# Kernel optimization log

Measured on AMD Instinct MI355X. Metric: run time of the kernel, lower is better.

## Reference

```python
import jax, jax.numpy as jnp
import numpy as np

PS = 7        # patch (window) size
DIM = 192     # channels
HEADS = 8
HID = 768     # mlp hidden = 4*dim
B = 8
HH = 112
WW = 112
EPS = 1e-5


def _rel_pos_index(ps):
    coords = np.stack(np.meshgrid(np.arange(ps), np.arange(ps), indexing='ij'))
    cf = coords.reshape(2, -1)
    rel = (cf[:, :, None] - cf[:, None, :]).transpose(1, 2, 0).astype(np.int64)
    rel[:, :, 0] += ps - 1
    rel[:, :, 1] += ps - 1
    rel[:, :, 0] *= 2 * ps - 1
    return rel.sum(-1)  # (N, N)

REL_IDX = jnp.asarray(_rel_pos_index(PS))  # (49, 49) int


def layer_norm(x, g, b):
    m = jnp.mean(x, axis=-1, keepdims=True)
    v = jnp.var(x, axis=-1, keepdims=True)
    return (x - m) * jax.lax.rsqrt(v + EPS) * g + b


def setup_inputs() -> dict:
    key = jax.random.key(0)
    ks = jax.random.split(key, 8)
    s = 0.02
    return {
        'x': jax.random.normal(ks[0], (B, HH * WW, DIM), jnp.float32),
        'norm1_g': jnp.ones((DIM,), jnp.float32),
        'norm1_b': jnp.zeros((DIM,), jnp.float32),
        'q_w': jax.random.normal(ks[1], (DIM, DIM), jnp.float32) * s,
        'q_b': jnp.zeros((DIM,), jnp.float32),
        'kv_w': jax.random.normal(ks[2], (2 * DIM, DIM), jnp.float32) * s,
        'kv_b': jnp.zeros((2 * DIM,), jnp.float32),
        'rpe_table': jax.random.normal(ks[3], ((2 * PS - 1) ** 2, HEADS), jnp.float32) * s,
        'proj_w': jax.random.normal(ks[4], (DIM, DIM), jnp.float32) * s,
        'proj_b': jnp.zeros((DIM,), jnp.float32),
        'norm2_g': jnp.ones((DIM,), jnp.float32),
        'norm2_b': jnp.zeros((DIM,), jnp.float32),
        'fc1_w': jax.random.normal(ks[5], (HID, DIM), jnp.float32) * s,
        'fc1_b': jnp.zeros((HID,), jnp.float32),
        'dw_w': jax.random.normal(ks[6], (HID, 1, 3, 3), jnp.float32) * s,
        'dw_b': jnp.zeros((HID,), jnp.float32),
        'fc2_w': jax.random.normal(ks[7], (DIM, HID), jnp.float32) * s,
        'fc2_b': jnp.zeros((DIM,), jnp.float32),
        'H': HH,
        'W': WW,
    }


def reference(x, norm1_g, norm1_b, q_w, q_b, kv_w, kv_b, rpe_table,
              proj_w, proj_b, norm2_g, norm2_b, fc1_w, fc1_b, dw_w, dw_b,
              fc2_w, fc2_b, H, W):
    Bsz, L, C = x.shape
    N = PS * PS
    hd = C // HEADS
    scale = hd ** -0.5
    nh, nw = H // PS, W // PS  # H, W chosen divisible by PS -> no padding

    shortcut = x
    xn = layer_norm(x, norm1_g, norm1_b)
    xi = xn.reshape(Bsz, H, W, C)
    # partition into non-overlapping PS x PS windows: (B*nP, N, C)
    p = xi.reshape(Bsz, nh, PS, nw, PS, C).transpose(0, 1, 3, 2, 4, 5).reshape(-1, N, C)

    # IPSA window attention (memory == x, T = 1)
    q = (p @ q_w.T + q_b).reshape(-1, N, HEADS, hd).transpose(0, 2, 1, 3) * scale
    kv = (p @ kv_w.T + kv_b).reshape(-1, N, 2, HEADS, hd).transpose(2, 0, 3, 1, 4)
    k, v = kv[0], kv[1]  # (B_, heads, N, hd)
    attn = jnp.einsum('bhnd,bhmd->bhnm', q, k)
    bias = rpe_table[REL_IDX.reshape(-1)].reshape(N, N, HEADS).transpose(2, 0, 1)
    attn = jax.nn.softmax(attn + bias[None], axis=-1)
    out = jnp.einsum('bhnm,bhmd->bhnd', attn, v).transpose(0, 2, 1, 3).reshape(-1, N, C)
    out = out @ proj_w.T + proj_b
    # reverse window partition back to (B, L, C)
    out = out.reshape(Bsz, nh, nw, PS, PS, C).transpose(0, 1, 3, 2, 4, 5).reshape(Bsz, L, C)
    x = shortcut + out

    # MLP with depthwise conv
    y = layer_norm(x, norm2_g, norm2_b)
    y = y @ fc1_w.T + fc1_b  # (B, L, HID)
    yc = y.transpose(0, 2, 1).reshape(Bsz, HID, H, W)
    yc = jax.lax.conv_general_dilated(
        yc, dw_w, window_strides=(1, 1), padding=((1, 1), (1, 1)),
        dimension_numbers=('NCHW', 'OIHW', 'NCHW'), feature_group_count=HID,
    ) + dw_b[None, :, None, None]
    y = yc.reshape(Bsz, HID, L).transpose(0, 2, 1)
    y = jax.nn.gelu(y, approximate=False)
    y = y @ fc2_w.T + fc2_b
    return x + y
```

## Files before the change

### kernel.cpp

```cpp
#include <hip/hip_runtime.h>
#include <hip/hip_bf16.h>
#include <cmath>

#define C_DIM 192
#define HID 768

typedef __attribute__((ext_vector_type(8))) __bf16 bf16x8;
typedef __attribute__((ext_vector_type(4))) float f32x4;

__device__ __forceinline__ void gload_lds16(const void* g, void* l) {
  __builtin_amdgcn_global_load_lds(
      (__attribute__((address_space(1))) void*)(const_cast<void*>(g)),
      (__attribute__((address_space(3))) void*)(l), 16, 0, 0);
}

__device__ __forceinline__ float bfu2f(ushort u) {
  return __uint_as_float((unsigned)u << 16);
}
__device__ __forceinline__ ushort f2bfu(float f) {
  __hip_bfloat16 h = __float2bfloat16(f);
  return *reinterpret_cast<ushort*>(&h);
}
__device__ __forceinline__ float fgelu(float x) {
  float z = x * (1.5957691216f + 0.071354816f * x * x);
  return x / (1.f + __expf(-z));
}

__global__ __launch_bounds__(256) void prep_kernel(
    const float* __restrict__ q_w, const float* __restrict__ q_b,
    const float* __restrict__ kv_w, const float* __restrict__ kv_b,
    const float* __restrict__ proj_w, const float* __restrict__ fc1_w,
    const float* __restrict__ fc2_w,
    __hip_bfloat16* __restrict__ wcat, float* __restrict__ bcat,
    __hip_bfloat16* __restrict__ projw, __hip_bfloat16* __restrict__ fc1w,
    __hip_bfloat16* __restrict__ fc2w)
{
  int idx = blockIdx.x * 256 + threadIdx.x;
  const float scale = 0.20412414523193154f;
  if (idx < 110592) {
    float v = (idx < 36864) ? q_w[idx] * scale : kv_w[idx - 36864];
    wcat[idx] = __float2bfloat16(v);
  }
  if (idx < 576) bcat[idx] = (idx < 192) ? q_b[idx] * scale : kv_b[idx - 192];
  if (idx < 36864) projw[idx] = __float2bfloat16(proj_w[idx]);
  if (idx < 147456) {
    fc1w[idx] = __float2bfloat16(fc1_w[idx]);
    fc2w[idx] = __float2bfloat16(fc2_w[idx]);
  }
}

__global__ __launch_bounds__(256) void ln_kernel(
    const float* __restrict__ x, const float* __restrict__ g,
    const float* __restrict__ b, __hip_bfloat16* __restrict__ out)
{
  int t = blockIdx.x * 4 + (threadIdx.x >> 6);
  int lane = threadIdx.x & 63;
  const float* xr = x + (size_t)t * C_DIM;
  float v0 = xr[lane], v1 = xr[lane + 64], v2 = xr[lane + 128];
  float s = v0 + v1 + v2;
  float sq = v0 * v0 + v1 * v1 + v2 * v2;
  #pragma unroll
  for (int off = 32; off > 0; off >>= 1) {
    s += __shfl_xor(s, off, 64);
    sq += __shfl_xor(sq, off, 64);
  }
  float mean = s * (1.0f / 192.0f);
  float var = sq * (1.0f / 192.0f) - mean * mean;
  float rstd = rsqrtf(var + 1e-5f);
  size_t o = (size_t)t * C_DIM;
  out[o + lane]       = __float2bfloat16((v0 - mean) * rstd * g[lane] + b[lane]);
  out[o + lane + 64]  = __float2bfloat16((v1 - mean) * rstd * g[lane + 64] + b[lane + 64]);
  out[o + lane + 128] = __float2bfloat16((v2 - mean) * rstd * g[lane + 128] + b[lane + 128]);
}

template <int EPI>
__global__ __launch_bounds__(256) void gemmA_kernel(
    const ushort* __restrict__ X, int lda, const ushort* __restrict__ W,
    const float* __restrict__ bias, const float* __restrict__ addin,
    void* __restrict__ outp, int N)
{
  __shared__ __align__(16) ushort Al[128 * 192];
  __shared__ __align__(16) ushort Bl[64 * 192];
  const int tid = threadIdx.x;
  const int lane = tid & 63;
  const int wv = tid >> 6;
  const int quad = lane >> 4;
  const int m15 = lane & 15;
  const long mBase = (long)blockIdx.y * 128;
  const int NT = N >> 6;

  #pragma unroll
  for (int r = 0; r < 12; ++r) {
    int sI = tid + r * 256;
    int row = sI / 24;
    int cs = sI - row * 24;
    int gc = cs - (row % 24); if (gc < 0) gc += 24;
    gload_lds16(X + (mBase + row) * (long)lda + gc * 8, Al + sI * 8);
  }

  const int rA0 = wv * 32 + m15, rA1 = rA0 + 16;
  const int rA0m = rA0 % 24, rA1m = rA1 % 24;

  for (int nt = 0; nt < NT; ++nt) {
    __syncthreads();
    #pragma unroll
    for (int r = 0; r < 6; ++r) {
      int sI = tid + r * 256;
      int row = sI / 24;
      int cs = sI - row * 24;
      int gc = cs - (row % 24); if (gc < 0) gc += 24;
      gload_lds16(W + (long)(nt * 64 + row) * 192 + gc * 8, Bl + sI * 8);
    }
    __syncthreads();

    f32x4 acc[2][4];
    #pragma unroll
    for (int r = 0; r < 2; ++r)
      #pragma unroll
      for (int c = 0; c < 4; ++c) acc[r][c] = (f32x4){0.f, 0.f, 0.f, 0.f};

    #pragma unroll
    for (int ks = 0; ks < 6; ++ks) {
      const int l = ks * 4 + quad;
      int pa0 = l + rA0m; if (pa0 >= 24) pa0 -= 24;
      int pa1 = l + rA1m; if (pa1 >= 24) pa1 -= 24;
      bf16x8 a0 = *(const bf16x8*)&Al[rA0 * 192 + pa0 * 8];
      bf16x8 a1 = *(const bf16x8*)&Al[rA1 * 192 + pa1 * 8];
      #pragma unroll
      for (int ct = 0; ct < 4; ++ct) {
        const int rB = ct * 16 + m15;
        int pb = l + (rB % 24); if (pb >= 24) pb -= 24;
        bf16x8 b = *(const bf16x8*)&Bl[rB * 192 + pb * 8];
        acc[0][ct] = __builtin_amdgcn_mfma_f32_16x16x32_bf16(a0, b, acc[0][ct], 0, 0, 0);
        acc[1][ct] = __builtin_amdgcn_mfma_f32_16x16x32_bf16(a1, b, acc[1][ct], 0, 0, 0);
      }
    }
    #pragma unroll
    for (int rt = 0; rt < 2; ++rt)
      #pragma unroll
      for (int ct = 0; ct < 4; ++ct)
        #pragma unroll
        for (int i = 0; i < 4; ++i) {
          long row = mBase + wv * 32 + rt * 16 + quad * 4 + i;
          int col = nt * 64 + ct * 16 + m15;
          float v = acc[rt][ct][i] + bias[col];
          if (EPI == 1) {
            v += addin[row * N + col];
            ((float*)outp)[row * N + col] = v;
          } else {
            ((__hip_bfloat16*)outp)[row * N + col] = __float2bfloat16(v);
          }
        }
  }
}

__global__ __launch_bounds__(256) void gemmB_kernel(
    const ushort* __restrict__ X, const ushort* __restrict__ W,
    const float* __restrict__ bias, const float* __restrict__ addin,
    float* __restrict__ outp)
{
  __shared__ __align__(16) ushort Al[128 * 192];
  __shared__ __align__(16) ushort Bl[64 * 192];
  const int tid = threadIdx.x;
  const int lane = tid & 63;
  const int wv = tid >> 6;
  const int quad = lane >> 4;
  const int m15 = lane & 15;
  const long mBase = (long)blockIdx.y * 128;

  const int rA0 = wv * 32 + m15, rA1 = rA0 + 16;
  const int rA0m = rA0 % 24, rA1m = rA1 % 24;

  f32x4 acc[3][2][4];
  #pragma unroll
  for (int n = 0; n < 3; ++n)
    #pragma unroll
    for (int r = 0; r < 2; ++r)
      #pragma unroll
      for (int c = 0; c < 4; ++c) acc[n][r][c] = (f32x4){0.f, 0.f, 0.f, 0.f};

  for (int kc = 0; kc < 4; ++kc) {
    for (int nt = 0; nt < 3; ++nt) {
      __syncthreads();
      if (nt == 0) {
        #pragma unroll
        for (int r = 0; r < 12; ++r) {
          int sI = tid + r * 256;
          int row = sI / 24;
          int cs = sI - row * 24;
          int gc = cs - (row % 24); if (gc < 0) gc += 24;
          gload_lds16(X + (mBase + row) * 768l + kc * 192 + gc * 8, Al + sI * 8);
        }
      }
      #pragma unroll
      for (int r = 0; r < 6; ++r) {
        int sI = tid + r * 256;
        int row = sI / 24;
        int cs = sI - row * 24;
        int gc = cs - (row % 24); if (gc < 0) gc += 24;
        gload_lds16(W + (long)(nt * 64 + row) * 768 + kc * 192 + gc * 8, Bl + sI * 8);
      }
      __syncthreads();
      #pragma unroll
      for (int ks = 0; ks < 6; ++ks) {
        const int l = ks * 4 + quad;
        int pa0 = l + rA0m; if (pa0 >= 24) pa0 -= 24;
        int pa1 = l + rA1m; if (pa1 >= 24) pa1 -= 24;
        bf16x8 a0 = *(const bf16x8*)&Al[rA0 * 192 + pa0 * 8];
        bf16x8 a1 = *(const bf16x8*)&Al[rA1 * 192 + pa1 * 8];
        #pragma unroll
        for (int ct = 0; ct < 4; ++ct) {
          const int rB = ct * 16 + m15;
          int pb = l + (rB % 24); if (pb >= 24) pb -= 24;
          bf16x8 b = *(const bf16x8*)&Bl[rB * 192 + pb * 8];
          acc[nt][0][ct] = __builtin_amdgcn_mfma_f32_16x16x32_bf16(a0, b, acc[nt][0][ct], 0, 0, 0);
          acc[nt][1][ct] = __builtin_amdgcn_mfma_f32_16x16x32_bf16(a1, b, acc[nt][1][ct], 0, 0, 0);
        }
      }
    }
  }
  #pragma unroll
  for (int nt = 0; nt < 3; ++nt)
    #pragma unroll
    for (int rt = 0; rt < 2; ++rt)
      #pragma unroll
      for (int ct = 0; ct < 4; ++ct)
        #pragma unroll
        for (int i = 0; i < 4; ++i) {
          long row = mBase + wv * 32 + rt * 16 + quad * 4 + i;
          int col = nt * 64 + ct * 16 + m15;
          float v = acc[nt][rt][ct][i] + bias[col] + addin[row * 192 + col];
          outp[row * 192 + col] = v;
        }
}

__global__ __launch_bounds__(256) void attn_kernel(
    const float* __restrict__ rpe, __hip_bfloat16* __restrict__ qkv)
{
  __shared__ float lds[4 * 2352 + 4 * 172];
  const int tid = threadIdx.x;
  const int lane = tid & 63;
  const int wv = tid >> 6;
  const int wh = blockIdx.x * 4 + wv;
  const int h = wh & 7;
  const int win = wh >> 3;
  const int b = win >> 8;
  const int wl = win & 255;
  const int whi = wl >> 4;
  const int wwi = wl & 15;
  ushort* qkv_u = (ushort*)qkv;
  float* kv_w = &lds[wv * 2352];
  float* bias_w = &lds[4 * 2352 + wv * 172];

  const long rowbase = (long)b * 12544 + (long)(whi * 7) * 112 + wwi * 7;

  #pragma unroll
  for (int rnd = 0; rnd < 10; ++rnd) {
    int e = lane + rnd * 64;
    if (e < 588) {
      int t = e / 12;
      int r = e - t * 12;
      int mat = r / 6;
      int d4 = (r - mat * 6) * 4;
      int py = t / 7, px = t - py * 7;
      long row = rowbase + py * 112 + px;
      ushort4 u = *(const ushort4*)(qkv_u + row * 576 + 192 + mat * 192 + h * 24 + d4);
      float* dst = kv_w + mat * 1176 + t * 24 + d4;
      dst[0] = bfu2f(u.x); dst[1] = bfu2f(u.y);
      dst[2] = bfu2f(u.z); dst[3] = bfu2f(u.w);
    }
  }
  for (int r = lane; r < 169; r += 64) bias_w[r] = rpe[r * 8 + h];
  __syncthreads();

  const int i = (lane < 49) ? lane : 48;
  const int yi = i / 7, xi = i - yi * 7;
  const int base_i = yi * 13 + xi + 84;
  const long myrow = rowbase + yi * 112 + xi;

  float q[24];
  #pragma unroll
  for (int d4 = 0; d4 < 24; d4 += 4) {
    ushort4 u = *(const ushort4*)(qkv_u + myrow * 576 + h * 24 + d4);
    q[d4] = bfu2f(u.x); q[d4 + 1] = bfu2f(u.y);
    q[d4 + 2] = bfu2f(u.z); q[d4 + 3] = bfu2f(u.w);
  }

  float s[49];
  #pragma unroll
  for (int j = 0; j < 49; ++j) {
    const int yj = j / 7, xj = j % 7;
    const int base_j = yj * 13 + xj;
    const float* kr = kv_w + j * 24;
    float acc = 0.f;
    #pragma unroll
    for (int d4 = 0; d4 < 24; d4 += 4) {
      f32x4 kk = *(const f32x4*)(kr + d4);
      acc += q[d4] * kk[0] + q[d4 + 1] * kk[1] + q[d4 + 2] * kk[2] + q[d4 + 3] * kk[3];
    }
    s[j] = acc + bias_w[base_i - base_j];
  }

  float mx = s[0];
  #pragma unroll
  for (int j = 1; j < 49; ++j) mx = fmaxf(mx, s[j]);
  float sm = 0.f;
  #pragma unroll
  for (int j = 0; j < 49; ++j) { s[j] = __expf(s[j] - mx); sm += s[j]; }
  const float inv = 1.f / sm;
  #pragma unroll
  for (int j = 0; j < 49; ++j) s[j] *= inv;

  float o[24];
  #pragma unroll
  for (int d = 0; d < 24; ++d) o[d] = 0.f;
  #pragma unroll
  for (int j = 0; j < 49; ++j) {
    const float p = s[j];
    const float* vr = kv_w + 1176 + j * 24;
    #pragma unroll
    for (int d4 = 0; d4 < 24; d4 += 4) {
      f32x4 vvv = *(const f32x4*)(vr + d4);
      o[d4] += p * vvv[0]; o[d4 + 1] += p * vvv[1];
      o[d4 + 2] += p * vvv[2]; o[d4 + 3] += p * vvv[3];
    }
  }

  if (lane < 49) {
    #pragma unroll
    for (int d4 = 0; d4 < 24; d4 += 4) {
      ushort4 u;
      u.x = f2bfu(o[d4]); u.y = f2bfu(o[d4 + 1]);
      u.z = f2bfu(o[d4 + 2]); u.w = f2bfu(o[d4 + 3]);
      *(ushort4*)(qkv_u + myrow * 576 + h * 24 + d4) = u;
    }
  }
}

__global__ __launch_bounds__(192) void dwconv_gelu_kernel(
    const ushort* __restrict__ y1, const float* __restrict__ w,
    const float* __restrict__ bias, ushort* __restrict__ y2)
{
  const int c = threadIdx.x * 4;
  const int w0 = blockIdx.y * 2;
  const int b = blockIdx.z;
  const int h0 = blockIdx.x * 28;

  float wt[9][4];
  #pragma unroll
  for (int k = 0; k < 9; ++k)
    #pragma unroll
    for (int j = 0; j < 4; ++j) wt[k][j] = w[(c + j) * 9 + k];
  float bs[4];
  #pragma unroll
  for (int j = 0; j < 4; ++j) bs[j] = bias[c + j];

  const bool okL = (w0 > 0), okR = (w0 + 2 < 112);
  ushort4 rb[6][4];

  auto loadrow = [&](int h, ushort4 dst[4]) {
    const ushort4 z = {0, 0, 0, 0};
    if (h < 0 || h >= 112) {
      dst[0] = z; dst[1] = z; dst[2] = z; dst[3] = z;
      return;
    }
    const ushort* p = y1 + (((size_t)(b * 112 + h)) * 112 + w0) * HID + c;
    dst[0] = okL ? *(const ushort4*)(p - HID) : z;
    dst[1] = *(const ushort4*)(p);
    dst[2] = *(const ushort4*)(p + HID);
    dst[3] = okR ? *(const ushort4*)(p + 2 * HID) : z;
  };

  loadrow(h0 - 1, rb[0]);
  loadrow(h0, rb[1]);

  for (int m = 0; m < 7; ++m) {
    const int hb = h0 + m * 4;
    loadrow(hb + 1, rb[2]);
    loadrow(hb + 2, rb[3]);
    loadrow(hb + 3, rb[4]);
    loadrow(hb + 4, rb[5]);
    #pragma unroll
    for (int o = 0; o < 4; ++o) {
      float acc0[4], acc1[4];
      #pragma unroll
      for (int j = 0; j < 4; ++j) { acc0[j] = bs[j]; acc1[j] = bs[j]; }
      #pragma unroll
      for (int dy = 0; dy < 3; ++dy) {
        float col[4][4];
        #pragma unroll
        for (int x = 0; x < 4; ++x) {
          ushort4 u = rb[o + dy][x];
          col[x][0] = bfu2f(u.x); col[x][1] = bfu2f(u.y);
          col[x][2] = bfu2f(u.z); col[x][3] = bfu2f(u.w);
        }
        #pragma unroll
        for (int dx = 0; dx < 3; ++dx)
          #pragma unroll
          for (int j = 0; j < 4; ++j) {
            acc0[j] += wt[dy * 3 + dx][j] * col[dx][j];
            acc1[j] += wt[dy * 3 + dx][j] * col[dx + 1][j];
          }
      }
      ushort* outp = y2 + (((size_t)(b * 112 + hb + o)) * 112 + w0) * HID + c;
      ushort4 o0, o1;
      o0.x = f2bfu(fgelu(acc0[0])); o0.y = f2bfu(fgelu(acc0[1]));
      o0.z = f2bfu(fgelu(acc0[2])); o0.w = f2bfu(fgelu(acc0[3]));
      o1.x = f2bfu(fgelu(acc1[0])); o1.y = f2bfu(fgelu(acc1[1]));
      o1.z = f2bfu(fgelu(acc1[2])); o1.w = f2bfu(fgelu(acc1[3]));
      *(ushort4*)(outp) = o0;
      *(ushort4*)(outp + HID) = o1;
    }
    #pragma unroll
    for (int x = 0; x < 4; ++x) {
      rb[0][x] = rb[4][x];
      rb[1][x] = rb[5][x];
    }
  }
}

extern "C" void kernel_launch(void* const* d_in, const int* in_sizes, int n_in,
                              void* d_out, int out_size, void* d_ws, size_t ws_size,
                              hipStream_t stream) {
  const float* x      = (const float*)d_in[0];
  const float* n1g    = (const float*)d_in[1];
  const float* n1b    = (const float*)d_in[2];
  const float* q_w    = (const float*)d_in[3];
  const float* q_b    = (const float*)d_in[4];
  const float* kv_w   = (const float*)d_in[5];
  const float* kv_b   = (const float*)d_in[6];
  const float* rpe    = (const float*)d_in[7];
  const float* proj_w = (const float*)d_in[8];
  const float* proj_b = (const float*)d_in[9];
  const float* n2g    = (const float*)d_in[10];
  const float* n2b    = (const float*)d_in[11];
  const float* fc1_w  = (const float*)d_in[12];
  const float* fc1_b  = (const float*)d_in[13];
  const float* dw_w   = (const float*)d_in[14];
  const float* dw_b   = (const float*)d_in[15];
  const float* fc2_w  = (const float*)d_in[16];
  const float* fc2_b  = (const float*)d_in[17];
  float* out = (float*)d_out;

  char* ws = (char*)d_ws;
  __hip_bfloat16* wcat  = (__hip_bfloat16*)(ws);
  __hip_bfloat16* projw = (__hip_bfloat16*)(ws + 221184);
  __hip_bfloat16* fc1w  = (__hip_bfloat16*)(ws + 294912);
  __hip_bfloat16* fc2w  = (__hip_bfloat16*)(ws + 589824);
  float* bcat           = (float*)(ws + 884736);
  const size_t WOFF = 1u << 20;

  int CB = 8;
  while (CB > 1 && WOFF + (size_t)CB * 12544 * 3456 > ws_size) CB >>= 1;
  const size_t Mc = (size_t)CB * 12544;
  char* Abuf = ws + WOFF;
  char* Bbuf = Abuf + Mc * 384;
  char* Cbuf = Bbuf + Mc * 1536;
  __hip_bfloat16* xn  = (__hip_bfloat16*)Abuf;
  __hip_bfloat16* qkv = (__hip_bfloat16*)Bbuf;
  __hip_bfloat16* y2  = (__hip_bfloat16*)Bbuf;
  __hip_bfloat16* y1  = (__hip_bfloat16*)Cbuf;

  prep_kernel<<<576, 256, 0, stream>>>(q_w, q_b, kv_w, kv_b, proj_w, fc1_w,
                                       fc2_w, wcat, bcat, projw, fc1w, fc2w);

  const int nChunks = 8 / CB;
  const int mt = CB * 98;
  for (int cchunk = 0; cchunk < nChunks; ++cchunk) {
    const size_t toff = (size_t)cchunk * Mc;
    const float* xc = x + toff * C_DIM;
    float* oc = out + toff * C_DIM;

    ln_kernel<<<(int)(Mc / 4), 256, 0, stream>>>(xc, n1g, n1b, xn);
    gemmA_kernel<0><<<dim3(1, mt), 256, 0, stream>>>(
        (const ushort*)xn, 192, (const ushort*)wcat, bcat, nullptr, qkv, 576);
    attn_kernel<<<CB * 512, 256, 0, stream>>>(rpe, qkv);
    gemmA_kernel<1><<<dim3(1, mt), 256, 0, stream>>>(
        (const ushort*)qkv, 576, (const ushort*)projw, proj_b, xc, oc, 192);
    ln_kernel<<<(int)(Mc / 4), 256, 0, stream>>>(oc, n2g, n2b, xn);
    gemmA_kernel<0><<<dim3(1, mt), 256, 0, stream>>>(
        (const ushort*)xn, 192, (const ushort*)fc1w, fc1_b, nullptr, y1, 768);
    dwconv_gelu_kernel<<<dim3(4, 56, CB), 192, 0, stream>>>(
        (const ushort*)y1, dw_w, dw_b, (ushort*)y2);
    gemmB_kernel<<<dim3(1, mt), 256, 0, stream>>>(
        (const ushort*)y2, (const ushort*)fc2w, fc2_b, oc, oc);
  }
}
```

Measured before the change: 660.5 us.

## Fuse proj GEMM with residual and LayerNorm2; vectorize attention math as float2

Adds a proj GEMM kernel in which each block computes all 192 output columns for its 128 rows. This lets the epilogue add the residual, write x, and compute the row LayerNorm through wave shuffles, writing the normalized bf16 activations directly. The separate ln_kernel launch and its re-read of x are removed. The attention kernel also switches to packed float2 arithmetic and splits the max/sum reductions into four chains to expose more ILP. Risks: higher register pressure from holding 96 accumulators plus per-column params, and a single-pass variance formula that is less numerically robust.

```diff
diff --git a/kernel.cpp b/kernel.cpp
--- a/kernel.cpp
+++ b/kernel.cpp
@@ -7,6 +7,7 @@
 
 typedef __attribute__((ext_vector_type(8))) __bf16 bf16x8;
 typedef __attribute__((ext_vector_type(4))) float f32x4;
+typedef __attribute__((ext_vector_type(2))) float f32x2;
 
 __device__ __forceinline__ void gload_lds16(const void* g, void* l) {
   __builtin_amdgcn_global_load_lds(
@@ -152,6 +153,137 @@
           }
         }
   }
+}
+
+__global__ __launch_bounds__(256) void gemmA_ln_kernel(
+    const ushort* __restrict__ X, int lda, const ushort* __restrict__ W,
+    const float* __restrict__ bias, const float* __restrict__ addin,
+    float* __restrict__ outp, const float* __restrict__ lng,
+    const float* __restrict__ lnb, __hip_bfloat16* __restrict__ xnout)
+{
+  __shared__ __align__(16) ushort Al[128 * 192];
+  __shared__ __align__(16) ushort Bl[64 * 192];
+  const int tid = threadIdx.x;
+  const int lane = tid & 63;
+  const int wv = tid >> 6;
+  const int quad = lane >> 4;
+  const int m15 = lane & 15;
+  const long mBase = (long)blockIdx.y * 128;
+
+  #pragma unroll
+  for (int r = 0; r < 12; ++r) {
+    int sI = tid + r * 256;
+    int row = sI / 24;
+    int cs = sI - row * 24;
+    int gc = cs - (row % 24); if (gc < 0) gc += 24;
+    gload_lds16(X + (mBase + row) * (long)lda + gc * 8, Al + sI * 8);
+  }
+
+  const int rA0 = wv * 32 + m15, rA1 = rA0 + 16;
+  const int rA0m = rA0 % 24, rA1m = rA1 % 24;
+
+  f32x4 acc[3][2][4];
+  #pragma unroll
+  for (int n = 0; n < 3; ++n)
+    #pragma unroll
+    for (int r = 0; r < 2; ++r)
+      #pragma unroll
+      for (int c = 0; c < 4; ++c) acc[n][r][c] = (f32x4){0.f, 0.f, 0.f, 0.f};
+
+  #pragma unroll
+  for (int nt = 0; nt < 3; ++nt) {
+    __syncthreads();
+    #pragma unroll
+    for (int r = 0; r < 6; ++r) {
+      int sI = tid + r * 256;
+      int row = sI / 24;
+      int cs = sI - row * 24;
+      int gc = cs - (row % 24); if (gc < 0) gc += 24;
+      gload_lds16(W + (long)(nt * 64 + row) * 192 + gc * 8, Bl + sI * 8);
+    }
+    __syncthreads();
+    #pragma unroll
+    for (int ks = 0; ks < 6; ++ks) {
+      const int l = ks * 4 + quad;
+      int pa0 = l + rA0m; if (pa0 >= 24) pa0 -= 24;
+      int pa1 = l + rA1m; if (pa1 >= 24) pa1 -= 24;
+      bf16x8 a0 = *(const bf16x8*)&Al[rA0 * 192 + pa0 * 8];
+      bf16x8 a1 = *(const bf16x8*)&Al[rA1 * 192 + pa1 * 8];
+      #pragma unroll
+      for (int ct = 0; ct < 4; ++ct) {
+        const int rB = ct * 16 + m15;
+        int pb = l + (rB % 24); if (pb >= 24) pb -= 24;
+        bf16x8 b = *(const bf16x8*)&Bl[rB * 192 + pb * 8];
+        acc[nt][0][ct] = __builtin_amdgcn_mfma_f32_16x16x32_bf16(a0, b, acc[nt][0][ct], 0, 0, 0);
+        acc[nt][1][ct] = __builtin_amdgcn_mfma_f32_16x16x32_bf16(a1, b, acc[nt][1][ct], 0, 0, 0);
+      }
+    }
+  }
+
+  float cb[12], cg[12], cbb[12];
+  #pragma unroll
+  for (int nt = 0; nt < 3; ++nt)
+    #pragma unroll
+    for (int ct = 0; ct < 4; ++ct) {
+      int col = nt * 64 + ct * 16 + m15;
+      cb[nt * 4 + ct] = bias[col];
+      cg[nt * 4 + ct] = lng[col];
+      cbb[nt * 4 + ct] = lnb[col];
+    }
+
+  float sum_[2][4], sq_[2][4];
+  #pragma unroll
+  for (int rt = 0; rt < 2; ++rt)
+    #pragma unroll
+    for (int i = 0; i < 4; ++i) { sum_[rt][i] = 0.f; sq_[rt][i] = 0.f; }
+
+  #pragma unroll
+  for (int nt = 0; nt < 3; ++nt)
+    #pragma unroll
+    for (int rt = 0; rt < 2; ++rt)
+      #pragma unroll
+      for (int ct = 0; ct < 4; ++ct)
+        #pragma unroll
+        for (int i = 0; i < 4; ++i) {
+          long row = mBase + wv * 32 + rt * 16 + quad * 4 + i;
+          int col = nt * 64 + ct * 16 + m15;
+          float v = acc[nt][rt][ct][i] + cb[nt * 4 + ct] + addin[row * 192 + col];
+          outp[row * 192 + col] = v;
+          acc[nt][rt][ct][i] = v;
+          sum_[rt][i] += v;
+          sq_[rt][i] += v * v;
+        }
+
+  float mean_[2][4], rstd_[2][4];
+  #pragma unroll
+  for (int rt = 0; rt < 2; ++rt)
+    #pragma unroll
+    for (int i = 0; i < 4; ++i) {
+      float s = sum_[rt][i], q = sq_[rt][i];
+      #pragma unroll
+      for (int m = 1; m < 16; m <<= 1) {
+        s += __shfl_xor(s, m, 64);
+        q += __shfl_xor(q, m, 64);
+      }
+      float mean = s * (1.0f / 192.0f);
+      mean_[rt][i] = mean;
+      rstd_[rt][i] = rsqrtf(q * (1.0f / 192.0f) - mean * mean + 1e-5f);
+    }
+
+  #pragma unroll
+  for (int nt = 0; nt < 3; ++nt)
+    #pragma unroll
+    for (int rt = 0; rt < 2; ++rt)
+      #pragma unroll
+      for (int ct = 0; ct < 4; ++ct)
+        #pragma unroll
+        for (int i = 0; i < 4; ++i) {
+          long row = mBase + wv * 32 + rt * 16 + quad * 4 + i;
+          int col = nt * 64 + ct * 16 + m15;
+          float v = (acc[nt][rt][ct][i] - mean_[rt][i]) * rstd_[rt][i] *
+                        cg[nt * 4 + ct] + cbb[nt * 4 + ct];
+          xnout[row * 192 + col] = __float2bfloat16(v);
+        }
 }
 
 __global__ __launch_bounds__(256) void gemmB_kernel(
@@ -278,12 +410,12 @@
   const int base_i = yi * 13 + xi + 84;
   const long myrow = rowbase + yi * 112 + xi;
 
-  float q[24];
+  f32x2 q2[12];
   #pragma unroll
   for (int d4 = 0; d4 < 24; d4 += 4) {
     ushort4 u = *(const ushort4*)(qkv_u + myrow * 576 + h * 24 + d4);
-    q[d4] = bfu2f(u.x); q[d4 + 1] = bfu2f(u.y);
-    q[d4 + 2] = bfu2f(u.z); q[d4 + 3] = bfu2f(u.w);
+    q2[(d4 >> 1)]     = (f32x2){bfu2f(u.x), bfu2f(u.y)};
+    q2[(d4 >> 1) + 1] = (f32x2){bfu2f(u.z), bfu2f(u.w)};
   }
 
   float s[49];
@@ -292,37 +424,51 @@
     const int yj = j / 7, xj = j % 7;
     const int base_j = yj * 13 + xj;
     const float* kr = kv_w + j * 24;
-    float acc = 0.f;
+    f32x2 a2 = {0.f, 0.f};
     #pragma unroll
     for (int d4 = 0; d4 < 24; d4 += 4) {
       f32x4 kk = *(const f32x4*)(kr + d4);
-      acc += q[d4] * kk[0] + q[d4 + 1] * kk[1] + q[d4 + 2] * kk[2] + q[d4 + 3] * kk[3];
-    }
-    s[j] = acc + bias_w[base_i - base_j];
-  }
-
-  float mx = s[0];
-  #pragma unroll
-  for (int j = 1; j < 49; ++j) mx = fmaxf(mx, s[j]);
-  float sm = 0.f;
-  #pragma unroll
-  for (int j = 0; j < 49; ++j) { s[j] = __expf(s[j] - mx); sm += s[j]; }
-  const float inv = 1.f / sm;
+      f32x2 klo = __builtin_shufflevector(kk, kk, 0, 1);
+      f32x2 khi = __builtin_shufflevector(kk, kk, 2, 3);
+      a2 += q2[(d4 >> 1)] * klo;
+      a2 += q2[(d4 >> 1) + 1] * khi;
+    }
+    s[j] = a2[0] + a2[1] + bias_w[base_i - base_j];
+  }
+
+  float m0 = fmaxf(s[0], s[48]);
+  float m1 = s[1], m2 = s[2], m3 = s[3];
+  #pragma unroll
+  for (int j = 4; j < 48; j += 4) {
+    m0 = fmaxf(m0, s[j]);     m1 = fmaxf(m1, s[j + 1]);
+    m2 = fmaxf(m2, s[j + 2]); m3 = fmaxf(m3, s[j + 3]);
+  }
+  const float mx = fmaxf(fmaxf(m0, m1), fmaxf(m2, m3));
+
+  #pragma unroll
+  for (int j = 0; j < 49; ++j) s[j] = __expf(s[j] - mx);
+
+  float t0 = s[48], t1 = 0.f, t2 = 0.f, t3 = 0.f;
+  #pragma unroll
+  for (int j = 0; j < 48; j += 4) {
+    t0 += s[j]; t1 += s[j + 1]; t2 += s[j + 2]; t3 += s[j + 3];
+  }
+  const float inv = 1.f / ((t0 + t1) + (t2 + t3));
   #pragma unroll
   for (int j = 0; j < 49; ++j) s[j] *= inv;
 
-  float o[24];
-  #pragma unroll
-  for (int d = 0; d < 24; ++d) o[d] = 0.f;
+  f32x2 o2[12];
+  #pragma unroll
+  for (int dd = 0; dd < 12; ++dd) o2[dd] = (f32x2){0.f, 0.f};
   #pragma unroll
   for (int j = 0; j < 49; ++j) {
-    const float p = s[j];
+    const f32x2 p2 = {s[j], s[j]};
     const float* vr = kv_w + 1176 + j * 24;
     #pragma unroll
     for (int d4 = 0; d4 < 24; d4 += 4) {
-      f32x4 vvv = *(const f32x4*)(vr + d4);
-      o[d4] += p * vvv[0]; o[d4 + 1] += p * vvv[1];
-      o[d4 + 2] += p * vvv[2]; o[d4 + 3] += p * vvv[3];
+      f32x4 vv = *(const f32x4*)(vr + d4);
+      o2[(d4 >> 1)]     += p2 * __builtin_shufflevector(vv, vv, 0, 1);
+      o2[(d4 >> 1) + 1] += p2 * __builtin_shufflevector(vv, vv, 2, 3);
     }
   }
 
@@ -330,8 +476,8 @@
     #pragma unroll
     for (int d4 = 0; d4 < 24; d4 += 4) {
       ushort4 u;
-      u.x = f2bfu(o[d4]); u.y = f2bfu(o[d4 + 1]);
-      u.z = f2bfu(o[d4 + 2]); u.w = f2bfu(o[d4 + 3]);
+      u.x = f2bfu(o2[(d4 >> 1)][0]);     u.y = f2bfu(o2[(d4 >> 1)][1]);
+      u.z = f2bfu(o2[(d4 >> 1) + 1][0]); u.w = f2bfu(o2[(d4 >> 1) + 1][1]);
       *(ushort4*)(qkv_u + myrow * 576 + h * 24 + d4) = u;
     }
   }
@@ -475,9 +621,9 @@
     gemmA_kernel<0><<<dim3(1, mt), 256, 0, stream>>>(
         (const ushort*)xn, 192, (const ushort*)wcat, bcat, nullptr, qkv, 576);
     attn_kernel<<<CB * 512, 256, 0, stream>>>(rpe, qkv);
-    gemmA_kernel<1><<<dim3(1, mt), 256, 0, stream>>>(
-        (const ushort*)qkv, 576, (const ushort*)projw, proj_b, xc, oc, 192);
-    ln_kernel<<<(int)(Mc / 4), 256, 0, stream>>>(oc, n2g, n2b, xn);
+    gemmA_ln_kernel<<<dim3(1, mt), 256, 0, stream>>>(
+        (const ushort*)qkv, 576, (const ushort*)projw, proj_b, xc, oc,
+        n2g, n2b, xn);
     gemmA_kernel<0><<<dim3(1, mt), 256, 0, stream>>>(
         (const ushort*)xn, 192, (const ushort*)fc1w, fc1_b, nullptr, y1, 768);
     dwconv_gelu_kernel<<<dim3(4, 56, CB), 192, 0, stream>>>(
```

Measured after the change: 822.5 us. +24.5%, slower.
